# Performance work log

Measured on AMD Instinct MI355X. Metric: run time of the kernel, lower is better.

## Reference

```python
import jax, jax.numpy as jnp
import numpy as np

B, S, C, D, SN = 32, 145, 768, 8192, 64

def setup_inputs() -> dict:
    key = jax.random.key(0)
    ks = jax.random.split(key, 12)
    h1 = jax.random.randint(ks[0], (C,), 0, D, dtype=jnp.int32)
    h2 = jax.random.randint(ks[1], (C,), 0, D, dtype=jnp.int32)
    s1 = jax.random.randint(ks[2], (C,), 0, 2, dtype=jnp.int32) * 2 - 1
    s2 = jax.random.randint(ks[3], (C,), 0, 2, dtype=jnp.int32) * 2 - 1
    return {
        'sensor': jax.random.normal(ks[4], (B, 1, SN), jnp.float32),
        'image_embeds': jax.random.normal(ks[5], (B, S, C), jnp.float32),
        'image_masks': jnp.ones((B, S), jnp.int32),
        'h1': h1, 'h2': h2, 's1': s1, 's2': s2,
        'd': D,
        'W_sensor': jax.random.normal(ks[6], (C, SN), jnp.float32) * 0.02,
        'b_sensor': jnp.zeros((C,), jnp.float32),
        'W_s2': jax.random.normal(ks[7], (S, 1), jnp.float32) * 0.02,
        'b_s2': jnp.zeros((S,), jnp.float32),
        'W_out': jax.random.normal(ks[8], (1, S), jnp.float32) * 0.02,
        'b_out': jnp.zeros((1,), jnp.float32),
        'tok_emb': jax.random.normal(ks[9], (2, C), jnp.float32) * 0.02,
    }

def _sketch(x, h, s, d):
    # count-sketch: scatter c channels into d bins with random signs
    v = x * s.astype(x.dtype)                      # [B,S,C]
    Q = jnp.zeros(x.shape[:2] + (d,), x.dtype)
    return Q.at[:, :, h].add(v)                    # duplicate hash indices accumulate

def _tsp(x, h1, h2, s1, s2, d):
    # FFT circular convolution of the two sketches
    F1 = jnp.fft.fft(_sketch(x, h1, s1, d))
    F2 = jnp.fft.fft(_sketch(x, h2, s2, d))
    return jnp.fft.ifft(F1 * F2).real              # [B,S,d]

def reference(sensor, image_embeds, image_masks, h1, h2, s1, s2, d,
              W_sensor, b_sensor, W_s2, b_s2, W_out, b_out, tok_emb):
    # sensor branch: [B,1,SN] -> [B,1,C] -> [B,C,1] -> [B,C,145] -> [B,145,C]
    se = sensor @ W_sensor.T + b_sensor
    se = jnp.swapaxes(se, 1, 2)
    se = se @ W_s2.T + b_s2
    se = jnp.swapaxes(se, 1, 2)
    # image branch: add token-type embedding (idx=1), masks define shape only
    img = image_embeds + tok_emb[1][None, None, :]
    z_x = _tsp(img, h1, h2, s1, s2, d)
    z_y = _tsp(se, h1, h2, s1, s2, d)
    ip = jnp.sum(z_x * z_y, axis=2)                # [B,S]
    bp = jnp.sign(ip) * jnp.sqrt(jnp.abs(ip) + 1e-5)
    norm = jnp.maximum(jnp.linalg.norm(bp, axis=1, keepdims=True), 1e-12)
    bp = bp / norm                                 # F.normalize p=2 dim=1
    out = bp @ W_out.T + b_out                     # [B,1]
    return out
```

## Files before the change

### kernel.cpp

```cpp
#include <hip/hip_runtime.h>
#include <hip/hip_bf16.h>
#include <math.h>

#define DD 8192
#define CC 768
#define SS 145
#define BB 32
#define SN 64
#define SROWS 160
#define NCKA 24

#define NETD 12
#define NCH 12
#define M01W 36
#define NWGD (BB*2*NETD)

#define ZT 512
#define NSL 16

typedef __attribute__((ext_vector_type(8))) short short8;
typedef __attribute__((ext_vector_type(4))) float f32x4;
typedef __attribute__((ext_vector_type(2))) float f32x2;

__device__ __forceinline__ void gload16(const void* g, void* l) {
    __builtin_amdgcn_global_load_lds(
        (const __attribute__((address_space(1))) unsigned int*)g,
        (__attribute__((address_space(3))) unsigned int*)l, 16, 0, 0);
}

__global__ __launch_bounds__(512) void kS(
    const float* __restrict__ sensor, const float* __restrict__ Wsen,
    const float* __restrict__ bsen,
    const int* __restrict__ h1, const int* __restrict__ h2,
    const int* __restrict__ s1, const int* __restrict__ s2,
    float4* __restrict__ CTG, float2* __restrict__ P2G)
{
    __shared__ float2 P2l[DD];
    __shared__ float  sens[SN];
    const int b   = blockIdx.x;
    const int tid = threadIdx.x;

    if (tid < SN) sens[tid] = sensor[b*SN + tid];
    {
        float4* p4 = (float4*)P2l;
        #pragma unroll
        for (int i = 0; i < 8; ++i) p4[tid + i*512] = make_float4(0.f,0.f,0.f,0.f);
    }
    __syncthreads();

    for (int c = tid; c < CC; c += 512) {
        float u = bsen[c];
        const float4* w = (const float4*)(Wsen + (size_t)c*SN);
        #pragma unroll
        for (int n4 = 0; n4 < 16; ++n4) {
            float4 wv = w[n4];
            u += sens[4*n4+0]*wv.x + sens[4*n4+1]*wv.y
               + sens[4*n4+2]*wv.z + sens[4*n4+3]*wv.w;
        }
        float f1 = (float)s1[c], f2 = (float)s2[c];
        float4 ct;
        ct.x = u * f1; ct.y = f1; ct.z = __int_as_float(h1[c] << 3); ct.w = 0.f;
        CTG[(size_t)b*CC + c] = ct;
        int t = h2[c];
        unsafeAtomicAdd(&P2l[t].x, u * f2);
        unsafeAtomicAdd(&P2l[t].y, f2);
    }
    __syncthreads();

    {
        const float4* p4 = (const float4*)P2l;
        float4* dst = (float4*)(P2G + (size_t)b*DD);
        #pragma unroll
        for (int i = 0; i < 8; ++i) dst[tid + i*512] = p4[tid + i*512];
    }
}

__global__ __launch_bounds__(ZT) void kZ(
    const float4* __restrict__ CTG, const float2* __restrict__ P2G,
    unsigned int* __restrict__ ZP, unsigned short* __restrict__ Z11b)
{
    __shared__ float2 P2l[DD];

    const int bid = blockIdx.x;
    const int wg  = (bid & 7)*(BB*NSL/8) + (bid >> 3);
    const int b   = wg >> 4;
    const int dsl = wg & (NSL-1);
    const int tid = threadIdx.x;
    const bool doZ11 = (b == 0);

    {
        const float4* src = (const float4*)(P2G + (size_t)b*DD);
        float4* dst = (float4*)P2l;
        #pragma unroll
        for (int i = 0; i < 8; ++i) dst[tid + i*ZT] = src[tid + i*ZT];
    }
    __syncthreads();

    const int d  = dsl*ZT + tid;
    const int d8 = d << 3;
    const float4* ctp = CTG + (size_t)b*CC;
    f32x2 accP = {0.f, 0.f};
    float accC2 = 0.f, acc1 = 0.f;
    #pragma unroll 4
    for (int c = 0; c < CC; ++c) {
        float4 ct = ctp[c];
        int ab = (d8 - __float_as_int(ct.z)) & 65535;
        f32x2 p = *(const f32x2*)((const char*)P2l + ab);
        f32x2 uu = {ct.x, ct.x};
        accP = __builtin_elementwise_fma(uu, p, accP);
        accC2 = fmaf(ct.y, p.x, accC2);
        if (doZ11) acc1 = fmaf(ct.y, p.y, acc1);
    }
    float accU = accP.x, accC = accP.y + accC2;

    __hip_bfloat16 zu = __float2bfloat16(accU);
    __hip_bfloat16 zc = __float2bfloat16(accC);
    ZP[(size_t)b*DD + d] = (unsigned int)*(unsigned short*)&zu
                         | ((unsigned int)*(unsigned short*)&zc << 16);
    if (doZ11) {
        __hip_bfloat16 z1 = __float2bfloat16(acc1);
        Z11b[d] = *(unsigned short*)&z1;
    }
}

__global__ __launch_bounds__(512) void kAM(
    const float* __restrict__ E, const float* __restrict__ tok,
    const int* __restrict__ s1, unsigned int* __restrict__ A1u,
    const unsigned short* __restrict__ Z11b,
    const int* __restrict__ h1, const int* __restrict__ h2,
    unsigned int* __restrict__ M11u)
{
    __shared__ unsigned short Z11l[DD];
    const int bid = blockIdx.x;
    const int tid = threadIdx.x;

    if (bid < 320) {
        if (tid < 384) {
            const int b  = bid / 10;
            const int r0 = (bid % 10) * 16;
            const int c  = 2*tid;
            const int ck = tid >> 4;
            const int c2 = tid & 15;
            const float s1a = (float)s1[c], s1b = (float)s1[c+1];
            const float ta = tok[CC + c] * s1a, tb = tok[CC + c + 1] * s1b;
            #pragma unroll
            for (int rr = 0; rr < 16; ++rr) {
                int row = r0 + rr;
                unsigned int word = 0;
                if (row < SS) {
                    float2 ev = *(const float2*)&E[((size_t)b*SS + row)*CC + c];
                    __hip_bfloat16 x0 = __float2bfloat16(ev.x*s1a + ta);
                    __hip_bfloat16 x1 = __float2bfloat16(ev.y*s1b + tb);
                    word = (unsigned int)*(unsigned short*)&x0
                         | ((unsigned int)*(unsigned short*)&x1 << 16);
                }
                int gp = (c2 >> 2) ^ (row & 3);
                A1u[((size_t)(b*NCKA + ck)*SROWS + row)*16 + gp*4 + (c2 & 3)] = word;
            }
        }
    } else {
        const int ck = bid - 320;
        {
            const uint4* src = (const uint4*)Z11b;
            uint4* dst = (uint4*)Z11l;
            #pragma unroll
            for (int i = 0; i < 2; ++i) dst[tid + i*512] = src[tid + i*512];
        }
        __syncthreads();

        #pragma unroll 4
        for (int i = 0; i < 24; ++i) {
            int idx = tid + i*512;
            int ep  = idx >> 4;
            int cpp = idx & 15;
            int ha = h1[ck*32 + 2*cpp];
            int hb = h1[ck*32 + 2*cpp + 1];
            int he = h2[ep];
            unsigned int lo = Z11l[(ha + he) & (DD-1)];
            unsigned int hi = Z11l[(hb + he) & (DD-1)];
            M11u[((size_t)ck*768 + ep)*16 + cpp] = lo | (hi << 16);
        }
    }
}

__global__ __launch_bounds__(512, 4) void kD(
    const unsigned int* __restrict__ A1u,
    const unsigned short* __restrict__ M11,
    const float* __restrict__ E, const float* __restrict__ tok,
    const int* __restrict__ h1, const int* __restrict__ h2,
    const int* __restrict__ s2,
    const float* __restrict__ Ws2, const float* __restrict__ bs2,
    const unsigned int* __restrict__ ZP, float* __restrict__ Q)
{
    __shared__ __align__(16) unsigned int   ZPl[DD];
    __shared__ __align__(16) unsigned short Lt[2][SROWS*32];
    __shared__ __align__(16) unsigned int   Mt01[2][64*M01W];
    __shared__ unsigned short h1l[CC];

    const int bid = blockIdx.x;
    const int wg  = (bid & 7)*(NWGD/8) + (bid >> 3);
    const int b   = wg / 24;
    const int r   = wg % 24;
    const int ch  = r / 12;
    const int et  = r % 12;
    const int tid = threadIdx.x;
    const int e0  = et * 64;
    const int cb0 = ch * 384;

    {
        const uint4* src = (const uint4*)(ZP + (size_t)b*DD);
        uint4* dst = (uint4*)ZPl;
        #pragma unroll
        for (int i = 0; i < 4; ++i) dst[tid + i*512] = src[tid + i*512];
    }
    for (int c = tid; c < CC; c += 512) h1l[c] = (unsigned short)h1[c];

    const int lane = tid & 63;
    const int wv   = tid >> 6;
    const int esub = wv & 3;
    const int shf  = wv >> 2;
    const int l15  = lane & 15;
    const int l4   = lane >> 4;
    const int eg   = e0 + esub*16 + l15;

    int gh2[4];
    #pragma unroll
    for (int j = 0; j < 4; ++j) gh2[j] = h2[e0 + ((tid + j*512) >> 5)];
    __syncthreads();

    const char* Abase = (const char*)A1u + (size_t)b*NCKA*SROWS*64;

#define STAGE_A(K, BUF) { \
    const char* cbase = Abase + (size_t)(ch*NCH + (K))*SROWS*64; \
    gload16(cbase + wv*1024 + lane*16, (char*)(BUF) + wv*1024); \
    if (wv < 2) \
        gload16(cbase + 8192 + wv*1024 + lane*16, \
                (char*)(BUF) + 8192 + wv*1024); \
    }

#define GATHER(K, MT) { \
    _Pragma("unroll") \
    for (int j = 0; j < 4; ++j) { \
        int idx = tid + j*512; \
        int ge = idx >> 5, gc = idx & 31; \
        int ad = ((int)h1l[cb0 + (K)*32 + gc] + gh2[j]) & (DD-1); \
        MT[ge*M01W + gc] = ZPl[ad]; \
    } }

#define LOADB2(K) \
    (*(const short8*)&M11[((size_t)(ch*NCH + (K))*768 + eg)*32 + l4*8])

#define MFMA_STEP(LT, MT, BQ) { \
    const unsigned int* mp = &MT[(esub*16 + l15)*M01W + l4*8]; \
    uint4 p0 = *(const uint4*)mp; \
    uint4 p1 = *(const uint4*)(mp + 4); \
    union { unsigned int u[4]; short8 s; } b0, b1; \
    b0.u[0] = (p0.x & 0xffffu) | (p0.y << 16); \
    b1.u[0] = (p0.x >> 16)     | (p0.y & 0xffff0000u); \
    b0.u[1] = (p0.z & 0xffffu) | (p0.w << 16); \
    b1.u[1] = (p0.z >> 16)     | (p0.w & 0xffff0000u); \
    b0.u[2] = (p1.x & 0xffffu) | (p1.y << 16); \
    b1.u[2] = (p1.x >> 16)     | (p1.y & 0xffff0000u); \
    b0.u[3] = (p1.z & 0xffffu) | (p1.w << 16); \
    b1.u[3] = (p1.z >> 16)     | (p1.w & 0xffff0000u); \
    _Pragma("unroll") \
    for (int t = 0; t < 5; ++t) { \
        int R = shf*80 + t*16 + l15; \
        short8 af = *(const short8*)&LT[R*32 + ((l4 ^ (R & 3))*8)]; \
        acc0[t] = __builtin_amdgcn_mfma_f32_16x16x32_bf16(af, b0.s, acc0[t], 0,0,0); \
        acc1[t] = __builtin_amdgcn_mfma_f32_16x16x32_bf16(af, b1.s, acc1[t], 0,0,0); \
        acc2[t] = __builtin_amdgcn_mfma_f32_16x16x32_bf16(af, BQ,   acc2[t], 0,0,0); \
    } }

    f32x4 acc0[5], acc1[5], acc2[5];
    #pragma unroll
    for (int t = 0; t < 5; ++t) {
        acc0[t] = (f32x4){0.f,0.f,0.f,0.f};
        acc1[t] = (f32x4){0.f,0.f,0.f,0.f};
        acc2[t] = (f32x4){0.f,0.f,0.f,0.f};
    }

    short8 bqA, bqB;
    STAGE_A(0, Lt[0])
    GATHER(0, Mt01[0])
    bqA = LOADB2(0);
    __syncthreads();

    #pragma unroll 1
    for (int k = 0; k < NCH; k += 2) {
        if (k + 1 < NCH) {
            STAGE_A(k + 1, Lt[1])
            GATHER(k + 1, Mt01[1])
            bqB = LOADB2(k + 1);
        }
        MFMA_STEP(Lt[0], Mt01[0], bqA)
        __syncthreads();

        if (k + 2 < NCH) {
            STAGE_A(k + 2, Lt[0])
            GATHER(k + 2, Mt01[0])
            bqA = LOADB2(k + 2);
        }
        if (k + 1 < NCH) {
            MFMA_STEP(Lt[1], Mt01[1], bqB)
        }
        __syncthreads();
    }
#undef STAGE_A
#undef GATHER
#undef LOADB2
#undef MFMA_STEP

    const float s2e = (float)s2[eg];
    const float t2e = tok[CC + eg] * s2e;
    #pragma unroll
    for (int t = 0; t < 5; ++t) {
        #pragma unroll
        for (int rr = 0; rr < 4; ++rr) {
            int s = shf*80 + t*16 + l4*4 + rr;
            float qv = 0.f;
            if (s < SS) {
                float a2v = E[((size_t)b*SS + s)*CC + eg] * s2e + t2e;
                float w2v = Ws2[s], bbv = bs2[s];
                qv = (w2v*w2v*acc0[t][rr] + w2v*bbv*acc1[t][rr]
                      + bbv*bbv*acc2[t][rr]) * a2v;
            }
            qv += __shfl_xor(qv, 1);
            qv += __shfl_xor(qv, 2);
            qv += __shfl_xor(qv, 4);
            qv += __shfl_xor(qv, 8);
            if (l15 == 0 && s < SS)
                unsafeAtomicAdd(&Q[b*SS + s], qv);
        }
    }
}

__global__ __launch_bounds__(256) void kE(
    const float* __restrict__ Q, const float* __restrict__ Wout,
    const float* __restrict__ bout, float* __restrict__ out)
{
    __shared__ float red[8];
    const int b = blockIdx.x, tid = threadIdx.x;
    float v = 0.f, w = 0.f;
    if (tid < SS) {
        float ip = Q[b*SS + tid];
        float sg = (ip > 0.f) ? 1.f : ((ip < 0.f) ? -1.f : 0.f);
        v = sg * sqrtf(fabsf(ip) + 1e-5f);
        w = v * Wout[tid];
    }
    float sq = v * v;
    #pragma unroll
    for (int off = 32; off > 0; off >>= 1) {
        sq += __shfl_down(sq, off, 64);
        w  += __shfl_down(w,  off, 64);
    }
    if ((tid & 63) == 0) { red[tid >> 6] = sq; red[4 + (tid >> 6)] = w; }
    __syncthreads();
    if (tid == 0) {
        float ssq  = red[0] + red[1] + red[2] + red[3];
        float sw   = red[4] + red[5] + red[6] + red[7];
        float norm = fmaxf(sqrtf(ssq), 1e-12f);
        out[b] = sw / norm + bout[0];
    }
}

extern "C" void kernel_launch(void* const* d_in, const int* in_sizes, int n_in,
                              void* d_out, int out_size, void* d_ws, size_t ws_size,
                              hipStream_t stream) {
    const float* sensor = (const float*)d_in[0];
    const float* E      = (const float*)d_in[1];
    const int*   h1     = (const int*)d_in[3];
    const int*   h2     = (const int*)d_in[4];
    const int*   s1     = (const int*)d_in[5];
    const int*   s2     = (const int*)d_in[6];
    const float* Wsen   = (const float*)d_in[8];
    const float* bsen   = (const float*)d_in[9];
    const float* Ws2    = (const float*)d_in[10];
    const float* bs2    = (const float*)d_in[11];
    const float* Wout   = (const float*)d_in[12];
    const float* bout   = (const float*)d_in[13];
    const float* tok    = (const float*)d_in[14];
    float* out = (float*)d_out;

    char* ws = (char*)d_ws;
    float4* CTG = (float4*)ws;
    float2* P2G = (float2*)(ws + (size_t)BB*CC*16);
    unsigned int* A1u = (unsigned int*)ws;
    const size_t A1_BYTES = (size_t)BB*NCKA*SROWS*64;
    unsigned int*   ZP   = (unsigned int*)(ws + A1_BYTES);
    unsigned short* Z11b = (unsigned short*)(ws + A1_BYTES + (size_t)BB*DD*4);
    unsigned int*   M11u = (unsigned int*)((char*)Z11b + (size_t)DD*2);
    float* Q = (float*)((char*)M11u + (size_t)NCKA*768*32*2);

    hipMemsetAsync(Q, 0, (size_t)BB*SS*sizeof(float), stream);

    kS<<<dim3(BB), dim3(512), 0, stream>>>(
        sensor, Wsen, bsen, h1, h2, s1, s2, CTG, P2G);

    kZ<<<dim3(BB*NSL), dim3(ZT), 0, stream>>>(CTG, P2G, ZP, Z11b);

    kAM<<<dim3(344), dim3(512), 0, stream>>>(
        E, tok, s1, A1u, Z11b, h1, h2, M11u);

    kD<<<dim3(NWGD), dim3(512), 0, stream>>>(
        A1u, (const unsigned short*)M11u, E, tok, h1, h2, s2, Ws2, bs2, ZP, Q);

    kE<<<dim3(BB), dim3(256), 0, stream>>>(Q, Wout, bout, out);
}
```

Baseline: 166.2 us.

## Fuse sensor sketch with A-packing, split M11 kernel, relax kD barriers

When the workspace is large enough, the sensor projection/sketch kernel is merged with the image-embedding bf16 packing into one launch, and Q is zeroed in-kernel instead of by a memset. The M11 gather moves into its own small kernel after kZ. The aim is to remove a launch and let the A-packing run alongside the sensor work. The kD pipeline replaces __syncthreads with a barrier that waits only for older vector-memory loads (vmcnt(1)), plus sched_barriers, so prefetches stay in flight across the barrier. This adds a correctness risk if the one outstanding load is one the next MFMA step needs, and it needs a larger workspace so the two buffers no longer alias.

Result: faster. 158.7 us (-4.5%).

```diff
diff --git a/kernel.cpp b/kernel.cpp
--- a/kernel.cpp
+++ b/kernel.cpp
@@ -28,18 +28,15 @@
         (__attribute__((address_space(3))) unsigned int*)l, 16, 0, 0);
 }
 
-__global__ __launch_bounds__(512) void kS(
+__device__ __forceinline__ void kS_body(
+    int b, int tid,
     const float* __restrict__ sensor, const float* __restrict__ Wsen,
     const float* __restrict__ bsen,
     const int* __restrict__ h1, const int* __restrict__ h2,
     const int* __restrict__ s1, const int* __restrict__ s2,
-    float4* __restrict__ CTG, float2* __restrict__ P2G)
-{
-    __shared__ float2 P2l[DD];
-    __shared__ float  sens[SN];
-    const int b   = blockIdx.x;
-    const int tid = threadIdx.x;
-
+    float4* __restrict__ CTG, float2* __restrict__ P2G, float2* P2l,
+    float* sens)
+{
     if (tid < SN) sens[tid] = sensor[b*SN + tid];
     {
         float4* p4 = (float4*)P2l;
@@ -73,6 +70,70 @@
         #pragma unroll
         for (int i = 0; i < 8; ++i) dst[tid + i*512] = p4[tid + i*512];
     }
+}
+
+__device__ __forceinline__ void kA_body(
+    int bid, int tid,
+    const float* __restrict__ E, const float* __restrict__ tok,
+    const int* __restrict__ s1, unsigned int* __restrict__ A1u)
+{
+    if (tid >= 384) return;
+    const int b  = bid / 10;
+    const int r0 = (bid % 10) * 16;
+    const int c  = 2*tid;
+    const int ck = tid >> 4;
+    const int c2 = tid & 15;
+    const float s1a = (float)s1[c], s1b = (float)s1[c+1];
+    const float ta = tok[CC + c] * s1a, tb = tok[CC + c + 1] * s1b;
+    #pragma unroll
+    for (int rr = 0; rr < 16; ++rr) {
+        int row = r0 + rr;
+        unsigned int word = 0;
+        if (row < SS) {
+            float2 ev = *(const float2*)&E[((size_t)b*SS + row)*CC + c];
+            __hip_bfloat16 x0 = __float2bfloat16(ev.x*s1a + ta);
+            __hip_bfloat16 x1 = __float2bfloat16(ev.y*s1b + tb);
+            word = (unsigned int)*(unsigned short*)&x0
+                 | ((unsigned int)*(unsigned short*)&x1 << 16);
+        }
+        int gp = (c2 >> 2) ^ (row & 3);
+        A1u[((size_t)(b*NCKA + ck)*SROWS + row)*16 + gp*4 + (c2 & 3)] = word;
+    }
+}
+
+__global__ __launch_bounds__(512) void kSA(
+    const float* __restrict__ sensor, const float* __restrict__ Wsen,
+    const float* __restrict__ bsen,
+    const int* __restrict__ h1, const int* __restrict__ h2,
+    const int* __restrict__ s1, const int* __restrict__ s2,
+    float4* __restrict__ CTG, float2* __restrict__ P2G,
+    const float* __restrict__ E, const float* __restrict__ tok,
+    unsigned int* __restrict__ A1u, float* __restrict__ Q)
+{
+    __shared__ float2 P2l[DD];
+    __shared__ float  sens[SN];
+    const int bid = blockIdx.x;
+    const int tid = threadIdx.x;
+    if (bid < 320) {
+        kA_body(bid, tid, E, tok, s1, A1u);
+    } else {
+        if (bid == 320) for (int i = tid; i < BB*SS; i += 512) Q[i] = 0.f;
+        kS_body(bid - 320, tid, sensor, Wsen, bsen, h1, h2, s1, s2,
+                CTG, P2G, P2l, sens);
+    }
+}
+
+__global__ __launch_bounds__(512) void kS(
+    const float* __restrict__ sensor, const float* __restrict__ Wsen,
+    const float* __restrict__ bsen,
+    const int* __restrict__ h1, const int* __restrict__ h2,
+    const int* __restrict__ s1, const int* __restrict__ s2,
+    float4* __restrict__ CTG, float2* __restrict__ P2G)
+{
+    __shared__ float2 P2l[DD];
+    __shared__ float  sens[SN];
+    kS_body(blockIdx.x, threadIdx.x, sensor, Wsen, bsen, h1, h2, s1, s2,
+            CTG, P2G, P2l, sens);
 }
 
 __global__ __launch_bounds__(ZT) void kZ(
@@ -123,6 +184,36 @@
     }
 }
 
+__global__ __launch_bounds__(512) void kM11(
+    const unsigned short* __restrict__ Z11b,
+    const int* __restrict__ h1, const int* __restrict__ h2,
+    unsigned int* __restrict__ M11u)
+{
+    __shared__ unsigned short Z11l[DD];
+    const int ck  = blockIdx.x;
+    const int tid = threadIdx.x;
+    {
+        const uint4* src = (const uint4*)Z11b;
+        uint4* dst = (uint4*)Z11l;
+        #pragma unroll
+        for (int i = 0; i < 2; ++i) dst[tid + i*512] = src[tid + i*512];
+    }
+    __syncthreads();
+
+    #pragma unroll 4
+    for (int i = 0; i < 24; ++i) {
+        int idx = tid + i*512;
+        int ep  = idx >> 4;
+        int cpp = idx & 15;
+        int ha = h1[ck*32 + 2*cpp];
+        int hb = h1[ck*32 + 2*cpp + 1];
+        int he = h2[ep];
+        unsigned int lo = Z11l[(ha + he) & (DD-1)];
+        unsigned int hi = Z11l[(hb + he) & (DD-1)];
+        M11u[((size_t)ck*768 + ep)*16 + cpp] = lo | (hi << 16);
+    }
+}
+
 __global__ __launch_bounds__(512) void kAM(
     const float* __restrict__ E, const float* __restrict__ tok,
     const int* __restrict__ s1, unsigned int* __restrict__ A1u,
@@ -133,31 +224,8 @@
     __shared__ unsigned short Z11l[DD];
     const int bid = blockIdx.x;
     const int tid = threadIdx.x;
-
     if (bid < 320) {
-        if (tid < 384) {
-            const int b  = bid / 10;
-            const int r0 = (bid % 10) * 16;
-            const int c  = 2*tid;
-            const int ck = tid >> 4;
-            const int c2 = tid & 15;
-            const float s1a = (float)s1[c], s1b = (float)s1[c+1];
-            const float ta = tok[CC + c] * s1a, tb = tok[CC + c + 1] * s1b;
-            #pragma unroll
-            for (int rr = 0; rr < 16; ++rr) {
-                int row = r0 + rr;
-                unsigned int word = 0;
-                if (row < SS) {
-                    float2 ev = *(const float2*)&E[((size_t)b*SS + row)*CC + c];
-                    __hip_bfloat16 x0 = __float2bfloat16(ev.x*s1a + ta);
-                    __hip_bfloat16 x1 = __float2bfloat16(ev.y*s1b + tb);
-                    word = (unsigned int)*(unsigned short*)&x0
-                         | ((unsigned int)*(unsigned short*)&x1 << 16);
-                }
-                int gp = (c2 >> 2) ^ (row & 3);
-                A1u[((size_t)(b*NCKA + ck)*SROWS + row)*16 + gp*4 + (c2 & 3)] = word;
-            }
-        }
+        kA_body(bid, tid, E, tok, s1, A1u);
     } else {
         const int ck = bid - 320;
         {
@@ -167,7 +235,6 @@
             for (int i = 0; i < 2; ++i) dst[tid + i*512] = src[tid + i*512];
         }
         __syncthreads();
-
         #pragma unroll 4
         for (int i = 0; i < 24; ++i) {
             int idx = tid + i*512;
@@ -229,6 +296,13 @@
     __syncthreads();
 
     const char* Abase = (const char*)A1u + (size_t)b*NCKA*SROWS*64;
+
+#define BARC() do { \
+    asm volatile("s_waitcnt vmcnt(1) lgkmcnt(0)" ::: "memory"); \
+    __builtin_amdgcn_sched_barrier(0); \
+    __builtin_amdgcn_s_barrier(); \
+    __builtin_amdgcn_sched_barrier(0); \
+} while (0)
 
 #define STAGE_A(K, BUF) { \
     const char* cbase = Abase + (size_t)(ch*NCH + (K))*SROWS*64; \
@@ -283,29 +357,33 @@
     short8 bqA, bqB;
     STAGE_A(0, Lt[0])
     GATHER(0, Mt01[0])
+    __builtin_amdgcn_sched_barrier(0);
     bqA = LOADB2(0);
-    __syncthreads();
+    BARC();
 
     #pragma unroll 1
     for (int k = 0; k < NCH; k += 2) {
         if (k + 1 < NCH) {
             STAGE_A(k + 1, Lt[1])
             GATHER(k + 1, Mt01[1])
+            __builtin_amdgcn_sched_barrier(0);
             bqB = LOADB2(k + 1);
         }
         MFMA_STEP(Lt[0], Mt01[0], bqA)
-        __syncthreads();
+        BARC();
 
         if (k + 2 < NCH) {
             STAGE_A(k + 2, Lt[0])
             GATHER(k + 2, Mt01[0])
+            __builtin_amdgcn_sched_barrier(0);
             bqA = LOADB2(k + 2);
         }
         if (k + 1 < NCH) {
             MFMA_STEP(Lt[1], Mt01[1], bqB)
         }
-        __syncthreads();
-    }
+        BARC();
+    }
+#undef BARC
 #undef STAGE_A
 #undef GATHER
 #undef LOADB2
@@ -383,27 +461,50 @@
     float* out = (float*)d_out;
 
     char* ws = (char*)d_ws;
-    float4* CTG = (float4*)ws;
-    float2* P2G = (float2*)(ws + (size_t)BB*CC*16);
-    unsigned int* A1u = (unsigned int*)ws;
-    const size_t A1_BYTES = (size_t)BB*NCKA*SROWS*64;
-    unsigned int*   ZP   = (unsigned int*)(ws + A1_BYTES);
-    unsigned short* Z11b = (unsigned short*)(ws + A1_BYTES + (size_t)BB*DD*4);
-    unsigned int*   M11u = (unsigned int*)((char*)Z11b + (size_t)DD*2);
-    float* Q = (float*)((char*)M11u + (size_t)NCKA*768*32*2);
-
-    hipMemsetAsync(Q, 0, (size_t)BB*SS*sizeof(float), stream);
-
-    kS<<<dim3(BB), dim3(512), 0, stream>>>(
-        sensor, Wsen, bsen, h1, h2, s1, s2, CTG, P2G);
-
-    kZ<<<dim3(BB*NSL), dim3(ZT), 0, stream>>>(CTG, P2G, ZP, Z11b);
-
-    kAM<<<dim3(344), dim3(512), 0, stream>>>(
-        E, tok, s1, A1u, Z11b, h1, h2, M11u);
-
-    kD<<<dim3(NWGD), dim3(512), 0, stream>>>(
-        A1u, (const unsigned short*)M11u, E, tok, h1, h2, s2, Ws2, bs2, ZP, Q);
-
-    kE<<<dim3(BB), dim3(256), 0, stream>>>(Q, Wout, bout, out);
-}
+    const size_t SZ_CTG = (size_t)BB*CC*16;
+    const size_t SZ_P2G = (size_t)BB*DD*8;
+    const size_t SZ_ZP  = (size_t)BB*DD*4;
+    const size_t SZ_Z11 = (size_t)DD*2;
+    const size_t SZ_M11 = (size_t)NCKA*768*64;
+    const size_t SZ_Q   = (size_t)BB*SS*4;
+    const size_t SZ_A1  = (size_t)BB*NCKA*SROWS*64;
+    const size_t needFused = SZ_CTG+SZ_P2G+SZ_ZP+SZ_Z11+SZ_M11+SZ_Q+SZ_A1;
+
+    if (ws_size >= needFused) {
+        float4* CTG = (float4*)ws;
+        float2* P2G = (float2*)(ws + SZ_CTG);
+        unsigned int*   ZP   = (unsigned int*)(ws + SZ_CTG + SZ_P2G);
+        unsigned short* Z11b = (unsigned short*)((char*)ZP + SZ_ZP);
+        unsigned int*   M11u = (unsigned int*)((char*)Z11b + SZ_Z11);
+        float*          Q    = (float*)((char*)M11u + SZ_M11);
+        unsigned int*   A1u  = (unsigned int*)((char*)Q + SZ_Q);
+
+        kSA<<<dim3(352), dim3(512), 0, stream>>>(
+            sensor, Wsen, bsen, h1, h2, s1, s2, CTG, P2G, E, tok, A1u, Q);
+        kZ<<<dim3(BB*NSL), dim3(ZT), 0, stream>>>(CTG, P2G, ZP, Z11b);
+        kM11<<<dim3(NCKA), dim3(512), 0, stream>>>(Z11b, h1, h2, M11u);
+        kD<<<dim3(NWGD), dim3(512), 0, stream>>>(
+            A1u, (const unsigned short*)M11u, E, tok, h1, h2, s2,
+            Ws2, bs2, ZP, Q);
+        kE<<<dim3(BB), dim3(256), 0, stream>>>(Q, Wout, bout, out);
+    } else {
+        float4* CTG = (float4*)ws;
+        float2* P2G = (float2*)(ws + SZ_CTG);
+        unsigned int* A1u = (unsigned int*)ws;
+        unsigned int*   ZP   = (unsigned int*)(ws + SZ_A1);
+        unsigned short* Z11b = (unsigned short*)(ws + SZ_A1 + SZ_ZP);
+        unsigned int*   M11u = (unsigned int*)((char*)Z11b + SZ_Z11);
+        float* Q = (float*)((char*)M11u + SZ_M11);
+
+        hipMemsetAsync(Q, 0, SZ_Q, stream);
+        kS<<<dim3(BB), dim3(512), 0, stream>>>(
+            sensor, Wsen, bsen, h1, h2, s1, s2, CTG, P2G);
+        kZ<<<dim3(BB*NSL), dim3(ZT), 0, stream>>>(CTG, P2G, ZP, Z11b);
+        kAM<<<dim3(344), dim3(512), 0, stream>>>(
+            E, tok, s1, A1u, Z11b, h1, h2, M11u);
+        kD<<<dim3(NWGD), dim3(512), 0, stream>>>(
+            A1u, (const unsigned short*)M11u, E, tok, h1, h2, s2,
+            Ws2, bs2, ZP, Q);
+        kE<<<dim3(BB), dim3(256), 0, stream>>>(Q, Wout, bout, out);
+    }
+}
```
